# Optimization experiments

Measured on AMD Instinct MI355X. Metric: run time of the kernel, lower is better.

## Reference

```python
import jax, jax.numpy as jnp
import numpy as np

B, L, D = 16, 4096, 512


def setup_inputs() -> dict:
    key = jax.random.key(0)
    ks = jax.random.split(key, 8)
    s = 1.0 / np.sqrt(D)
    x = jax.random.normal(ks[0], (B, L, D), dtype=jnp.float32)
    Wk = jax.random.normal(ks[1], (D, D), dtype=jnp.float32) * s
    Wq = jax.random.normal(ks[2], (D, D), dtype=jnp.float32) * s
    Wv = jax.random.normal(ks[3], (D, D), dtype=jnp.float32) * s
    bk = jnp.zeros((D,), jnp.float32)
    bq = jnp.zeros((D,), jnp.float32)
    bv = jnp.zeros((D,), jnp.float32)
    lens = jax.random.randint(ks[4], (B,), 1, L + 1, dtype=jnp.int32)
    return {"x": x, "Wk": Wk, "bk": bk, "Wq": Wq, "bq": bq,
            "Wv": Wv, "bv": bv, "lens": lens}


def reference(x, Wk, bk, Wq, bq, Wv, bv, lens):
    # Dropout is identity in eval mode.
    x_k = jnp.tanh(jnp.einsum('bld,ed->ble', x, Wk) + bk)  # [B,L,D]
    x_q = jnp.tanh(jnp.einsum('bld,ed->ble', x, Wq) + bq)
    x_v = jnp.tanh(jnp.einsum('bld,ed->ble', x, Wv) + bv)
    # sum_j (x_k_i . x_q_j) == x_k_i . sum_j x_q_j  (algebraic collapse of the L x L bmm)
    q_sum = x_q.sum(axis=1)                                # [B,D]
    w = jnp.einsum('bld,bd->bl', x_k, q_sum) / (D ** 0.5)  # [B,L]
    pad = jnp.arange(L)[None, :] >= lens[:, None]          # True at padding
    w = jnp.where(pad, -jnp.inf, w)
    w = jax.nn.softmax(w, axis=1)                          # [B,L]
    # (x_v * w[...,None]).sum(-1) == x_v.sum(-1) * w
    return x_v.sum(axis=-1) * w                            # [B,L]
```

## Files before the change

### kernel.cpp

```cpp
#include <hip/hip_runtime.h>
#include <hip/hip_bf16.h>
#include <math.h>

typedef __attribute__((ext_vector_type(8))) short short8;
typedef __attribute__((ext_vector_type(16))) float f32x16;
typedef __attribute__((ext_vector_type(4))) unsigned short us4;
typedef __attribute__((ext_vector_type(8))) unsigned short us8;

static __device__ __forceinline__ unsigned short bf16_rn(float f) {
  unsigned u = __float_as_uint(f);
  u += 0x7FFFu + ((u >> 16) & 1u);
  return (unsigned short)(u >> 16);
}
static __device__ __forceinline__ void cvt_hilo(float f, unsigned short& h, unsigned short& l) {
  unsigned u = __float_as_uint(f);
  unsigned hr = u + 0x7FFFu + ((u >> 16) & 1u);
  h = (unsigned short)(hr >> 16);
  l = bf16_rn(f - __uint_as_float(hr & 0xFFFF0000u));
}
static __device__ __forceinline__ float ftanh(float x) {
  float e = __builtin_amdgcn_exp2f(x * 2.885390081777927f);
  return 1.0f - 2.0f * __builtin_amdgcn_rcpf(e + 1.0f);
}

__global__ void prep_kernel(const float* __restrict__ Wq,
                            const float* __restrict__ Wk,
                            const float* __restrict__ Wv,
                            unsigned short* __restrict__ ws_u16) {
  int id = blockIdx.x * 256 + threadIdx.x;
  int mat = id >> 15;
  int rem = id & 32767;
  int fn = rem >> 11;
  int gk = (rem >> 6) & 31;
  int ln = rem & 63;
  int e  = fn * 32 + (ln & 31);
  int d0 = gk * 16 + ((ln >> 5) << 3);
  const float* W = (mat == 0) ? Wq : (mat == 1) ? Wk : Wv;
  unsigned short* oh = ws_u16 + (size_t)mat * 524288 + (size_t)rem * 8;
  unsigned short* ol = oh + 262144;
  const float* src = W + (size_t)e * 512 + d0;
#pragma unroll
  for (int j = 0; j < 8; ++j) {
    unsigned short h, l;
    cvt_hilo(src[j], h, l);
    oh[j] = h;
    ol[j] = l;
  }
}

__global__ __launch_bounds__(512, 2) void pass1_q(
    const float* __restrict__ x,
    const unsigned short* __restrict__ bh,
    const unsigned short* __restrict__ bl,
    const float* __restrict__ bias,
    float* __restrict__ qpart) {
  __shared__ unsigned short hib[2][128 * 40];
  __shared__ unsigned short lob[2][128 * 40];

  const int tid = threadIdx.x;
  const int lane = tid & 63;
  const int w = tid >> 6;
  const int l31 = lane & 31, hs = lane >> 5;
  const int sr = tid >> 2, sc = (tid & 3) * 8;
  const float* gxr = x + (size_t)blockIdx.x * 128 * 512 + (size_t)sr * 512 + sc;

  const int aoff = l31 * 40 + hs * 8;
  const unsigned short* bhp = bh + (size_t)w * 16384 + (size_t)lane * 8;
  const unsigned short* blp = bl + (size_t)w * 16384 + (size_t)lane * 8;

  f32x16 acc[4][2] = {};

#define STAGE1(BUFI, V0, V1)                                        \
  {                                                                 \
    float tf[8] = {(V0).x, (V0).y, (V0).z, (V0).w,                  \
                   (V1).x, (V1).y, (V1).z, (V1).w};                 \
    us8 hv, lv;                                                     \
    _Pragma("unroll")                                               \
    for (int j = 0; j < 8; ++j) {                                   \
      unsigned short hh, ll;                                        \
      cvt_hilo(tf[j], hh, ll);                                      \
      hv[j] = hh; lv[j] = ll;                                       \
    }                                                               \
    *(us8*)&hib[BUFI][sr * 40 + sc] = hv;                           \
    *(us8*)&lob[BUFI][sr * 40 + sc] = lv;                           \
  }

  float4 xa0 = *(const float4*)(gxr);
  float4 xa1 = *(const float4*)(gxr + 4);
  STAGE1(0, xa0, xa1)
  float4 xb0 = *(const float4*)(gxr + 32);
  float4 xb1 = *(const float4*)(gxr + 36);
  __syncthreads();

#pragma unroll 1
  for (int c = 0; c < 16; ++c) {
    const int cur = c & 1;
    if (c < 15) { STAGE1(cur ^ 1, xb0, xb1) }
    if (c < 14) {
      xb0 = *(const float4*)(gxr + (c + 2) * 32);
      xb1 = *(const float4*)(gxr + (c + 2) * 32 + 4);
    }
    __syncthreads();

    short8 Bh[2][2], Bl[2][2];
#pragma unroll
    for (int ks = 0; ks < 2; ++ks)
#pragma unroll
      for (int nn = 0; nn < 2; ++nn) {
        const int go = nn * (8 * 16384) + (c * 2 + ks) * 512;
        Bh[ks][nn] = *(const short8*)(bhp + go);
        Bl[ks][nn] = *(const short8*)(blp + go);
      }
    const unsigned short* hc = &hib[cur][0];
    const unsigned short* lc = &lob[cur][0];
#pragma unroll
    for (int ks = 0; ks < 2; ++ks) {
      short8 ah[4], al[4];
#pragma unroll
      for (int mt = 0; mt < 4; ++mt) {
        ah[mt] = *(const short8*)(hc + aoff + mt * 1280 + ks * 16);
        al[mt] = *(const short8*)(lc + aoff + mt * 1280 + ks * 16);
      }
#pragma unroll
      for (int nn = 0; nn < 2; ++nn)
#pragma unroll
        for (int mt = 0; mt < 4; ++mt) {
          acc[mt][nn] = __builtin_amdgcn_mfma_f32_32x32x16_bf16(ah[mt], Bh[ks][nn], acc[mt][nn], 0, 0, 0);
          acc[mt][nn] = __builtin_amdgcn_mfma_f32_32x32x16_bf16(al[mt], Bh[ks][nn], acc[mt][nn], 0, 0, 0);
          acc[mt][nn] = __builtin_amdgcn_mfma_f32_32x32x16_bf16(ah[mt], Bl[ks][nn], acc[mt][nn], 0, 0, 0);
        }
    }
    __syncthreads();
  }
#undef STAGE1

  float cs[2];
#pragma unroll
  for (int nn = 0; nn < 2; ++nn) {
    float bc = bias[(w + 8 * nn) * 32 + l31];
    float s = 0.f;
#pragma unroll
    for (int mt = 0; mt < 4; ++mt)
#pragma unroll
      for (int r = 0; r < 16; ++r)
        s += ftanh(acc[mt][nn][r] + bc);
    s += __shfl_xor(s, 32);
    cs[nn] = s;
  }
  if (lane < 32) {
#pragma unroll
    for (int nn = 0; nn < 2; ++nn)
      qpart[(size_t)blockIdx.x * 512 + (w + 8 * nn) * 32 + l31] = cs[nn];
  }
}

__global__ __launch_bounds__(512, 2) void pass2_kv(
    const float* __restrict__ x,
    const unsigned short* __restrict__ kh,
    const unsigned short* __restrict__ kl,
    const unsigned short* __restrict__ vh,
    const float* __restrict__ bk,
    const float* __restrict__ bv,
    const float* __restrict__ q_sum,
    float* __restrict__ scores,
    float* __restrict__ sv) {
  __shared__ unsigned short hib[2][64 * 40];
  __shared__ unsigned short lob[2][64 * 40];
  __shared__ float redk[8][64];
  __shared__ float redv[8][64];

  const int tid = threadIdx.x;
  const int lane = tid & 63;
  const int w = tid >> 6;
  const int l31 = lane & 31, hs = lane >> 5;
  const int sr = tid >> 3, sc = (tid & 7) * 4;
  const float* gxr = x + (size_t)blockIdx.x * 64 * 512 + (size_t)sr * 512 + sc;

  const int aoff = l31 * 40 + hs * 8;
  const unsigned short* khp = kh + (size_t)w * 16384 + (size_t)lane * 8;
  const unsigned short* klp = kl + (size_t)w * 16384 + (size_t)lane * 8;
  const unsigned short* vhp = vh + (size_t)w * 16384 + (size_t)lane * 8;

  f32x16 acck[2][2] = {};
  f32x16 accv[2][2] = {};

#define STAGE2(BUFI, V)                                             \
  {                                                                 \
    float tf[4] = {(V).x, (V).y, (V).z, (V).w};                     \
    us4 hv, lv;                                                     \
    _Pragma("unroll")                                               \
    for (int j = 0; j < 4; ++j) {                                   \
      unsigned short hh, ll;                                        \
      cvt_hilo(tf[j], hh, ll);                                      \
      hv[j] = hh; lv[j] = ll;                                       \
    }                                                               \
    *(us4*)&hib[BUFI][sr * 40 + sc] = hv;                           \
    *(us4*)&lob[BUFI][sr * 40 + sc] = lv;                           \
  }

  float4 xa = *(const float4*)(gxr);
  STAGE2(0, xa)
  float4 xb = *(const float4*)(gxr + 32);
  __syncthreads();

#pragma unroll 1
  for (int c = 0; c < 16; ++c) {
    const int cur = c & 1;
    if (c < 15) { STAGE2(cur ^ 1, xb) }
    if (c < 14) { xb = *(const float4*)(gxr + (c + 2) * 32); }
    __syncthreads();

    short8 Kh[2][2], Kl[2][2], Vh[2][2];
#pragma unroll
    for (int ks = 0; ks < 2; ++ks)
#pragma unroll
      for (int nn = 0; nn < 2; ++nn) {
        const int go = nn * (8 * 16384) + (c * 2 + ks) * 512;
        Kh[ks][nn] = *(const short8*)(khp + go);
        Kl[ks][nn] = *(const short8*)(klp + go);
        Vh[ks][nn] = *(const short8*)(vhp + go);
      }
    const unsigned short* hc = &hib[cur][0];
    const unsigned short* lc = &lob[cur][0];
#pragma unroll
    for (int ks = 0; ks < 2; ++ks) {
      short8 ah[2], al[2];
#pragma unroll
      for (int mt = 0; mt < 2; ++mt) {
        ah[mt] = *(const short8*)(hc + aoff + mt * 1280 + ks * 16);
        al[mt] = *(const short8*)(lc + aoff + mt * 1280 + ks * 16);
      }
#pragma unroll
      for (int nn = 0; nn < 2; ++nn)
#pragma unroll
        for (int mt = 0; mt < 2; ++mt) {
          acck[mt][nn] = __builtin_amdgcn_mfma_f32_32x32x16_bf16(ah[mt], Kh[ks][nn], acck[mt][nn], 0, 0, 0);
          acck[mt][nn] = __builtin_amdgcn_mfma_f32_32x32x16_bf16(al[mt], Kh[ks][nn], acck[mt][nn], 0, 0, 0);
          acck[mt][nn] = __builtin_amdgcn_mfma_f32_32x32x16_bf16(ah[mt], Kl[ks][nn], acck[mt][nn], 0, 0, 0);
          accv[mt][nn] = __builtin_amdgcn_mfma_f32_32x32x16_bf16(ah[mt], Vh[ks][nn], accv[mt][nn], 0, 0, 0);
        }
    }
    __syncthreads();
  }
#undef STAGE2

  const int b = blockIdx.x >> 6;
  float qs[2], bkc[2], bvc[2];
#pragma unroll
  for (int nn = 0; nn < 2; ++nn) {
    int col = (w + 8 * nn) * 32 + l31;
    qs[nn] = q_sum[b * 512 + col];
    bkc[nn] = bk[col];
    bvc[nn] = bv[col];
  }
#pragma unroll
  for (int mt = 0; mt < 2; ++mt)
#pragma unroll
    for (int r = 0; r < 16; ++r) {
      float sk = ftanh(acck[mt][0][r] + bkc[0]) * qs[0] +
                 ftanh(acck[mt][1][r] + bkc[1]) * qs[1];
      float s_v = ftanh(accv[mt][0][r] + bvc[0]) +
                  ftanh(accv[mt][1][r] + bvc[1]);
#pragma unroll
      for (int off = 1; off <= 16; off <<= 1) {
        sk += __shfl_xor(sk, off);
        s_v += __shfl_xor(s_v, off);
      }
      if (l31 == 0) {
        int row = mt * 32 + (r & 3) + 8 * (r >> 2) + 4 * hs;
        redk[w][row] = sk;
        redv[w][row] = s_v;
      }
    }
  __syncthreads();
  if (tid < 64) {
    float s = 0.f;
#pragma unroll
    for (int j = 0; j < 8; ++j) s += redk[j][tid];
    scores[(size_t)blockIdx.x * 64 + tid] = s;
  } else if (tid < 128) {
    int r = tid - 64;
    float s = 0.f;
#pragma unroll
    for (int j = 0; j < 8; ++j) s += redv[j][r];
    sv[(size_t)blockIdx.x * 64 + r] = s;
  }
}

__global__ void reduce_q(const float* __restrict__ qpart, float* __restrict__ q_sum) {
  int b = blockIdx.x;
  int e = threadIdx.x;
  const float* p = qpart + (size_t)b * 32 * 512 + e;
  float s = 0.f;
#pragma unroll
  for (int j = 0; j < 32; ++j) s += p[j * 512];
  q_sum[b * 512 + e] = s;
}

__global__ void softmax_out(const float* __restrict__ scores,
                            const float* __restrict__ sv,
                            const int* __restrict__ lens,
                            float* __restrict__ out) {
  const int b = blockIdx.x;
  const int tid = threadIdx.x;
  const int lane = tid & 63, wid = tid >> 6;
  const int len = lens[b];
  const float scale = 0.04419417382415922f;
  __shared__ float sb[4];
  __shared__ float sb2[4];

  float sreg[16];
  const float* sc = scores + (size_t)b * 4096;
#pragma unroll
  for (int j = 0; j < 16; ++j) sreg[j] = sc[tid + j * 256] * scale;

  float m = -1e30f;
#pragma unroll
  for (int j = 0; j < 16; ++j)
    if (tid + j * 256 < len) m = fmaxf(m, sreg[j]);
#pragma unroll
  for (int off = 32; off >= 1; off >>= 1) m = fmaxf(m, __shfl_xor(m, off));
  if (lane == 0) sb[wid] = m;
  __syncthreads();
  m = fmaxf(fmaxf(sb[0], sb[1]), fmaxf(sb[2], sb[3]));

  float s = 0.f;
#pragma unroll
  for (int j = 0; j < 16; ++j)
    if (tid + j * 256 < len) s += expf(sreg[j] - m);
#pragma unroll
  for (int off = 32; off >= 1; off >>= 1) s += __shfl_xor(s, off);
  if (lane == 0) sb2[wid] = s;
  __syncthreads();
  const float inv = 1.f / (sb2[0] + sb2[1] + sb2[2] + sb2[3]);

  const float* svb = sv + (size_t)b * 4096;
  float* ob = out + (size_t)b * 4096;
#pragma unroll
  for (int j = 0; j < 16; ++j) {
    int l = tid + j * 256;
    ob[l] = (l < len) ? svb[l] * expf(sreg[j] - m) * inv : 0.0f;
  }
}

extern "C" void kernel_launch(void* const* d_in, const int* in_sizes, int n_in,
                              void* d_out, int out_size, void* d_ws, size_t ws_size,
                              hipStream_t stream) {
  const float* x  = (const float*)d_in[0];
  const float* Wk = (const float*)d_in[1];
  const float* bk = (const float*)d_in[2];
  const float* Wq = (const float*)d_in[3];
  const float* bq = (const float*)d_in[4];
  const float* Wv = (const float*)d_in[5];
  const float* bv = (const float*)d_in[6];
  const int* lens = (const int*)d_in[7];
  float* out = (float*)d_out;

  char* ws = (char*)d_ws;
  unsigned short* wfu = (unsigned short*)ws;
  const size_t WQ_HI = 0, WQ_LO = 262144;
  const size_t WK_HI = 524288, WK_LO = 786432;
  const size_t WV_HI = 1048576;
  float* qpart  = (float*)(ws + 3u * 1024 * 1024);
  float* q_sum  = (float*)(ws + 5u * 1024 * 1024);
  float* sv     = (float*)(ws + 5u * 1024 * 1024 + 32768);
  float* scores = (float*)(ws + 5u * 1024 * 1024 + 32768 + 262144);

  prep_kernel<<<384, 256, 0, stream>>>(Wq, Wk, Wv, wfu);
  pass1_q<<<512, 512, 0, stream>>>(x, wfu + WQ_HI, wfu + WQ_LO, bq, qpart);
  reduce_q<<<16, 512, 0, stream>>>(qpart, q_sum);
  pass2_kv<<<1024, 512, 0, stream>>>(x, wfu + WK_HI, wfu + WK_LO, wfu + WV_HI,
                                     bk, bv, q_sum, scores, sv);
  softmax_out<<<16, 256, 0, stream>>>(scores, sv, lens, out);
}
```

Before: 271.9 us.

## Use triple-buffered LDS staging to drop one barrier per k-chunk

Both GEMM passes move from double-buffered to triple-buffered LDS tiles for the hi/lo bf16 split of x. The trailing __syncthreads in each k-loop iteration is removed. The conversion and store of the next chunk now happen after the weight loads and overlap with the MFMAs on the current buffer. This costs 50% more LDS per block, which may limit occupancy with two 512-thread blocks per CU, and the reordered global loads could change latency hiding.

New measurement: 263.3 us. 3.2% less time.

```diff
diff --git a/kernel.cpp b/kernel.cpp
--- a/kernel.cpp
+++ b/kernel.cpp
@@ -54,8 +54,8 @@
     const unsigned short* __restrict__ bl,
     const float* __restrict__ bias,
     float* __restrict__ qpart) {
-  __shared__ unsigned short hib[2][128 * 40];
-  __shared__ unsigned short lob[2][128 * 40];
+  __shared__ unsigned short hib[3][128 * 40];
+  __shared__ unsigned short lob[3][128 * 40];
 
   const int tid = threadIdx.x;
   const int lane = tid & 63;
@@ -85,23 +85,17 @@
     *(us8*)&lob[BUFI][sr * 40 + sc] = lv;                           \
   }
 
-  float4 xa0 = *(const float4*)(gxr);
-  float4 xa1 = *(const float4*)(gxr + 4);
-  STAGE1(0, xa0, xa1)
-  float4 xb0 = *(const float4*)(gxr + 32);
-  float4 xb1 = *(const float4*)(gxr + 36);
-  __syncthreads();
-
+  float4 xs0 = *(const float4*)(gxr);
+  float4 xs1 = *(const float4*)(gxr + 4);
+  STAGE1(0, xs0, xs1)
+  xs0 = *(const float4*)(gxr + 32);
+  xs1 = *(const float4*)(gxr + 36);
+
+  int cur = 0;
 #pragma unroll 1
   for (int c = 0; c < 16; ++c) {
-    const int cur = c & 1;
-    if (c < 15) { STAGE1(cur ^ 1, xb0, xb1) }
-    if (c < 14) {
-      xb0 = *(const float4*)(gxr + (c + 2) * 32);
-      xb1 = *(const float4*)(gxr + (c + 2) * 32 + 4);
-    }
+    const int nxt = (cur == 2) ? 0 : cur + 1;
     __syncthreads();
-
     short8 Bh[2][2], Bl[2][2];
 #pragma unroll
     for (int ks = 0; ks < 2; ++ks)
@@ -111,6 +105,13 @@
         Bh[ks][nn] = *(const short8*)(bhp + go);
         Bl[ks][nn] = *(const short8*)(blp + go);
       }
+    float4 xn0 = xs0, xn1 = xs1;
+    if (c < 14) {
+      xn0 = *(const float4*)(gxr + (c + 2) * 32);
+      xn1 = *(const float4*)(gxr + (c + 2) * 32 + 4);
+    }
+    if (c < 15) { STAGE1(nxt, xs0, xs1) }
+
     const unsigned short* hc = &hib[cur][0];
     const unsigned short* lc = &lob[cur][0];
 #pragma unroll
@@ -130,7 +131,8 @@
           acc[mt][nn] = __builtin_amdgcn_mfma_f32_32x32x16_bf16(ah[mt], Bl[ks][nn], acc[mt][nn], 0, 0, 0);
         }
     }
-    __syncthreads();
+    xs0 = xn0; xs1 = xn1;
+    cur = nxt;
   }
 #undef STAGE1
 
@@ -164,8 +166,8 @@
     const float* __restrict__ q_sum,
     float* __restrict__ scores,
     float* __restrict__ sv) {
-  __shared__ unsigned short hib[2][64 * 40];
-  __shared__ unsigned short lob[2][64 * 40];
+  __shared__ unsigned short hib[3][64 * 40];
+  __shared__ unsigned short lob[3][64 * 40];
   __shared__ float redk[8][64];
   __shared__ float redv[8][64];
 
@@ -198,18 +200,15 @@
     *(us4*)&lob[BUFI][sr * 40 + sc] = lv;                           \
   }
 
-  float4 xa = *(const float4*)(gxr);
-  STAGE2(0, xa)
-  float4 xb = *(const float4*)(gxr + 32);
-  __syncthreads();
-
+  float4 xs = *(const float4*)(gxr);
+  STAGE2(0, xs)
+  xs = *(const float4*)(gxr + 32);
+
+  int cur = 0;
 #pragma unroll 1
   for (int c = 0; c < 16; ++c) {
-    const int cur = c & 1;
-    if (c < 15) { STAGE2(cur ^ 1, xb) }
-    if (c < 14) { xb = *(const float4*)(gxr + (c + 2) * 32); }
+    const int nxt = (cur == 2) ? 0 : cur + 1;
     __syncthreads();
-
     short8 Kh[2][2], Kl[2][2], Vh[2][2];
 #pragma unroll
     for (int ks = 0; ks < 2; ++ks)
@@ -220,6 +219,10 @@
         Kl[ks][nn] = *(const short8*)(klp + go);
         Vh[ks][nn] = *(const short8*)(vhp + go);
       }
+    float4 xn = xs;
+    if (c < 14) { xn = *(const float4*)(gxr + (c + 2) * 32); }
+    if (c < 15) { STAGE2(nxt, xs) }
+
     const unsigned short* hc = &hib[cur][0];
     const unsigned short* lc = &lob[cur][0];
 #pragma unroll
@@ -240,7 +243,8 @@
           accv[mt][nn] = __builtin_amdgcn_mfma_f32_32x32x16_bf16(ah[mt], Vh[ks][nn], accv[mt][nn], 0, 0, 0);
         }
     }
-    __syncthreads();
+    xs = xn;
+    cur = nxt;
   }
 #undef STAGE2
 
```

## Stage full-K 32-row x tile in LDS and stream weights per wave

Applied to the files above, without the earlier changes.

Both GEMM passes now load a whole 32x512 row tile of x into LDS up front (hi/lo bf16 split, padded stride) and then run the full K loop with no per-chunk barriers. Each of 4 waves owns 4 output column tiles and streams weight fragments straight from global memory. Blocks shrink to 256 threads and grids grow to 2048, which gives more independent blocks and removes the double-buffer synchronisation. In exchange, weight reuse per block drops because each block covers only 32 rows, so weight traffic from L2 rises, and the LDS footprint per block grows.

Result: slower. 453.4 us (+66.7%).

```diff
diff --git a/kernel.cpp b/kernel.cpp
--- a/kernel.cpp
+++ b/kernel.cpp
@@ -2,10 +2,11 @@
 #include <hip/hip_bf16.h>
 #include <math.h>
 
+#define LSTRIDE 520
+
 typedef __attribute__((ext_vector_type(8))) short short8;
 typedef __attribute__((ext_vector_type(16))) float f32x16;
 typedef __attribute__((ext_vector_type(4))) unsigned short us4;
-typedef __attribute__((ext_vector_type(8))) unsigned short us8;
 
 static __device__ __forceinline__ unsigned short bf16_rn(float f) {
   unsigned u = __float_as_uint(f);
@@ -48,113 +49,80 @@
   }
 }
 
-__global__ __launch_bounds__(512, 2) void pass1_q(
+#define STAGE_TILE(GX)                                                      \
+  {                                                                         \
+    const int row = tid >> 3, cb = (tid & 7) * 4;                           \
+    const float* gsrc = (GX) + (size_t)row * 512 + cb;                      \
+    unsigned short* hd = &hib[row * LSTRIDE + cb];                          \
+    unsigned short* ld = &lob[row * LSTRIDE + cb];                          \
+    _Pragma("unroll")                                                       \
+    for (int j = 0; j < 16; ++j) {                                          \
+      float4 v = *(const float4*)(gsrc + j * 32);                           \
+      us4 hv, lv;                                                           \
+      unsigned short hh, ll;                                                \
+      cvt_hilo(v.x, hh, ll); hv[0] = hh; lv[0] = ll;                        \
+      cvt_hilo(v.y, hh, ll); hv[1] = hh; lv[1] = ll;                        \
+      cvt_hilo(v.z, hh, ll); hv[2] = hh; lv[2] = ll;                        \
+      cvt_hilo(v.w, hh, ll); hv[3] = hh; lv[3] = ll;                        \
+      *(us4*)(hd + j * 32) = hv;                                            \
+      *(us4*)(ld + j * 32) = lv;                                            \
+    }                                                                       \
+  }
+
+__global__ __launch_bounds__(256, 2) void pass1_q(
     const float* __restrict__ x,
     const unsigned short* __restrict__ bh,
     const unsigned short* __restrict__ bl,
     const float* __restrict__ bias,
     float* __restrict__ qpart) {
-  __shared__ unsigned short hib[2][128 * 40];
-  __shared__ unsigned short lob[2][128 * 40];
+  __shared__ unsigned short hib[32 * LSTRIDE];
+  __shared__ unsigned short lob[32 * LSTRIDE];
 
   const int tid = threadIdx.x;
   const int lane = tid & 63;
   const int w = tid >> 6;
   const int l31 = lane & 31, hs = lane >> 5;
-  const int sr = tid >> 2, sc = (tid & 3) * 8;
-  const float* gxr = x + (size_t)blockIdx.x * 128 * 512 + (size_t)sr * 512 + sc;
-
-  const int aoff = l31 * 40 + hs * 8;
-  const unsigned short* bhp = bh + (size_t)w * 16384 + (size_t)lane * 8;
-  const unsigned short* blp = bl + (size_t)w * 16384 + (size_t)lane * 8;
-
-  f32x16 acc[4][2] = {};
-
-#define STAGE1(BUFI, V0, V1)                                        \
-  {                                                                 \
-    float tf[8] = {(V0).x, (V0).y, (V0).z, (V0).w,                  \
-                   (V1).x, (V1).y, (V1).z, (V1).w};                 \
-    us8 hv, lv;                                                     \
-    _Pragma("unroll")                                               \
-    for (int j = 0; j < 8; ++j) {                                   \
-      unsigned short hh, ll;                                        \
-      cvt_hilo(tf[j], hh, ll);                                      \
-      hv[j] = hh; lv[j] = ll;                                       \
-    }                                                               \
-    *(us8*)&hib[BUFI][sr * 40 + sc] = hv;                           \
-    *(us8*)&lob[BUFI][sr * 40 + sc] = lv;                           \
-  }
-
-  float4 xa0 = *(const float4*)(gxr);
-  float4 xa1 = *(const float4*)(gxr + 4);
-  STAGE1(0, xa0, xa1)
-  float4 xb0 = *(const float4*)(gxr + 32);
-  float4 xb1 = *(const float4*)(gxr + 36);
-  __syncthreads();
-
-#pragma unroll 1
-  for (int c = 0; c < 16; ++c) {
-    const int cur = c & 1;
-    if (c < 15) { STAGE1(cur ^ 1, xb0, xb1) }
-    if (c < 14) {
-      xb0 = *(const float4*)(gxr + (c + 2) * 32);
-      xb1 = *(const float4*)(gxr + (c + 2) * 32 + 4);
-    }
-    __syncthreads();
-
-    short8 Bh[2][2], Bl[2][2];
-#pragma unroll
-    for (int ks = 0; ks < 2; ++ks)
-#pragma unroll
-      for (int nn = 0; nn < 2; ++nn) {
-        const int go = nn * (8 * 16384) + (c * 2 + ks) * 512;
-        Bh[ks][nn] = *(const short8*)(bhp + go);
-        Bl[ks][nn] = *(const short8*)(blp + go);
+
+  STAGE_TILE(x + (size_t)blockIdx.x * 32 * 512)
+  __syncthreads();
+
+  const unsigned short* bhp = bh + (size_t)lane * 8;
+  const unsigned short* blp = bl + (size_t)lane * 8;
+  const int abase = l31 * LSTRIDE + hs * 8;
+
+  f32x16 acc[4] = {};
+#pragma unroll 4
+  for (int kc = 0; kc < 16; ++kc) {
+#pragma unroll
+    for (int ks = 0; ks < 2; ++ks) {
+      short8 ah = *(const short8*)&hib[abase + kc * 32 + ks * 16];
+      short8 al = *(const short8*)&lob[abase + kc * 32 + ks * 16];
+      const int gk = kc * 2 + ks;
+#pragma unroll
+      for (int i = 0; i < 4; ++i) {
+        const int bo = ((w + i * 4) * 32 + gk) * 512;
+        short8 Bh = *(const short8*)(bhp + bo);
+        short8 Bl = *(const short8*)(blp + bo);
+        acc[i] = __builtin_amdgcn_mfma_f32_32x32x16_bf16(ah, Bh, acc[i], 0, 0, 0);
+        acc[i] = __builtin_amdgcn_mfma_f32_32x32x16_bf16(al, Bh, acc[i], 0, 0, 0);
+        acc[i] = __builtin_amdgcn_mfma_f32_32x32x16_bf16(ah, Bl, acc[i], 0, 0, 0);
       }
-    const unsigned short* hc = &hib[cur][0];
-    const unsigned short* lc = &lob[cur][0];
-#pragma unroll
-    for (int ks = 0; ks < 2; ++ks) {
-      short8 ah[4], al[4];
-#pragma unroll
-      for (int mt = 0; mt < 4; ++mt) {
-        ah[mt] = *(const short8*)(hc + aoff + mt * 1280 + ks * 16);
-        al[mt] = *(const short8*)(lc + aoff + mt * 1280 + ks * 16);
-      }
-#pragma unroll
-      for (int nn = 0; nn < 2; ++nn)
-#pragma unroll
-        for (int mt = 0; mt < 4; ++mt) {
-          acc[mt][nn] = __builtin_amdgcn_mfma_f32_32x32x16_bf16(ah[mt], Bh[ks][nn], acc[mt][nn], 0, 0, 0);
-          acc[mt][nn] = __builtin_amdgcn_mfma_f32_32x32x16_bf16(al[mt], Bh[ks][nn], acc[mt][nn], 0, 0, 0);
-          acc[mt][nn] = __builtin_amdgcn_mfma_f32_32x32x16_bf16(ah[mt], Bl[ks][nn], acc[mt][nn], 0, 0, 0);
-        }
-    }
-    __syncthreads();
-  }
-#undef STAGE1
-
-  float cs[2];
-#pragma unroll
-  for (int nn = 0; nn < 2; ++nn) {
-    float bc = bias[(w + 8 * nn) * 32 + l31];
+    }
+  }
+
+#pragma unroll
+  for (int i = 0; i < 4; ++i) {
+    const int n = w + i * 4;
+    float bc = bias[n * 32 + l31];
     float s = 0.f;
 #pragma unroll
-    for (int mt = 0; mt < 4; ++mt)
-#pragma unroll
-      for (int r = 0; r < 16; ++r)
-        s += ftanh(acc[mt][nn][r] + bc);
+    for (int r = 0; r < 16; ++r) s += ftanh(acc[i][r] + bc);
     s += __shfl_xor(s, 32);
-    cs[nn] = s;
-  }
-  if (lane < 32) {
-#pragma unroll
-    for (int nn = 0; nn < 2; ++nn)
-      qpart[(size_t)blockIdx.x * 512 + (w + 8 * nn) * 32 + l31] = cs[nn];
-  }
-}
-
-__global__ __launch_bounds__(512, 2) void pass2_kv(
+    if (lane < 32) qpart[(size_t)blockIdx.x * 512 + n * 32 + l31] = s;
+  }
+}
+
+__global__ __launch_bounds__(256, 2) void pass2_kv(
     const float* __restrict__ x,
     const unsigned short* __restrict__ kh,
     const unsigned short* __restrict__ kl,
@@ -164,137 +132,99 @@
     const float* __restrict__ q_sum,
     float* __restrict__ scores,
     float* __restrict__ sv) {
-  __shared__ unsigned short hib[2][64 * 40];
-  __shared__ unsigned short lob[2][64 * 40];
-  __shared__ float redk[8][64];
-  __shared__ float redv[8][64];
+  __shared__ unsigned short hib[32 * LSTRIDE];
+  __shared__ unsigned short lob[32 * LSTRIDE];
+  __shared__ float redk[4][32];
+  __shared__ float redv[4][32];
 
   const int tid = threadIdx.x;
   const int lane = tid & 63;
   const int w = tid >> 6;
   const int l31 = lane & 31, hs = lane >> 5;
-  const int sr = tid >> 3, sc = (tid & 7) * 4;
-  const float* gxr = x + (size_t)blockIdx.x * 64 * 512 + (size_t)sr * 512 + sc;
-
-  const int aoff = l31 * 40 + hs * 8;
-  const unsigned short* khp = kh + (size_t)w * 16384 + (size_t)lane * 8;
-  const unsigned short* klp = kl + (size_t)w * 16384 + (size_t)lane * 8;
-  const unsigned short* vhp = vh + (size_t)w * 16384 + (size_t)lane * 8;
-
-  f32x16 acck[2][2] = {};
-  f32x16 accv[2][2] = {};
-
-#define STAGE2(BUFI, V)                                             \
-  {                                                                 \
-    float tf[4] = {(V).x, (V).y, (V).z, (V).w};                     \
-    us4 hv, lv;                                                     \
-    _Pragma("unroll")                                               \
-    for (int j = 0; j < 4; ++j) {                                   \
-      unsigned short hh, ll;                                        \
-      cvt_hilo(tf[j], hh, ll);                                      \
-      hv[j] = hh; lv[j] = ll;                                       \
-    }                                                               \
-    *(us4*)&hib[BUFI][sr * 40 + sc] = hv;                           \
-    *(us4*)&lob[BUFI][sr * 40 + sc] = lv;                           \
-  }
-
-  float4 xa = *(const float4*)(gxr);
-  STAGE2(0, xa)
-  float4 xb = *(const float4*)(gxr + 32);
-  __syncthreads();
-
-#pragma unroll 1
-  for (int c = 0; c < 16; ++c) {
-    const int cur = c & 1;
-    if (c < 15) { STAGE2(cur ^ 1, xb) }
-    if (c < 14) { xb = *(const float4*)(gxr + (c + 2) * 32); }
-    __syncthreads();
-
-    short8 Kh[2][2], Kl[2][2], Vh[2][2];
-#pragma unroll
-    for (int ks = 0; ks < 2; ++ks)
-#pragma unroll
-      for (int nn = 0; nn < 2; ++nn) {
-        const int go = nn * (8 * 16384) + (c * 2 + ks) * 512;
-        Kh[ks][nn] = *(const short8*)(khp + go);
-        Kl[ks][nn] = *(const short8*)(klp + go);
-        Vh[ks][nn] = *(const short8*)(vhp + go);
+
+  STAGE_TILE(x + (size_t)blockIdx.x * 32 * 512)
+  __syncthreads();
+
+  const unsigned short* khp = kh + (size_t)lane * 8;
+  const unsigned short* klp = kl + (size_t)lane * 8;
+  const unsigned short* vhp = vh + (size_t)lane * 8;
+  const int abase = l31 * LSTRIDE + hs * 8;
+
+  f32x16 acck[4] = {};
+  f32x16 accv[4] = {};
+#pragma unroll 4
+  for (int kc = 0; kc < 16; ++kc) {
+#pragma unroll
+    for (int ks = 0; ks < 2; ++ks) {
+      short8 ah = *(const short8*)&hib[abase + kc * 32 + ks * 16];
+      short8 al = *(const short8*)&lob[abase + kc * 32 + ks * 16];
+      const int gk = kc * 2 + ks;
+#pragma unroll
+      for (int i = 0; i < 4; ++i) {
+        const int bo = ((w + i * 4) * 32 + gk) * 512;
+        short8 Kh = *(const short8*)(khp + bo);
+        short8 Kl = *(const short8*)(klp + bo);
+        short8 Vh = *(const short8*)(vhp + bo);
+        acck[i] = __builtin_amdgcn_mfma_f32_32x32x16_bf16(ah, Kh, acck[i], 0, 0, 0);
+        acck[i] = __builtin_amdgcn_mfma_f32_32x32x16_bf16(al, Kh, acck[i], 0, 0, 0);
+        acck[i] = __builtin_amdgcn_mfma_f32_32x32x16_bf16(ah, Kl, acck[i], 0, 0, 0);
+        accv[i] = __builtin_amdgcn_mfma_f32_32x32x16_bf16(ah, Vh, accv[i], 0, 0, 0);
       }
-    const unsigned short* hc = &hib[cur][0];
-    const unsigned short* lc = &lob[cur][0];
-#pragma unroll
-    for (int ks = 0; ks < 2; ++ks) {
-      short8 ah[2], al[2];
-#pragma unroll
-      for (int mt = 0; mt < 2; ++mt) {
-        ah[mt] = *(const short8*)(hc + aoff + mt * 1280 + ks * 16);
-        al[mt] = *(const short8*)(lc + aoff + mt * 1280 + ks * 16);
-      }
-#pragma unroll
-      for (int nn = 0; nn < 2; ++nn)
-#pragma unroll
-        for (int mt = 0; mt < 2; ++mt) {
-          acck[mt][nn] = __builtin_amdgcn_mfma_f32_32x32x16_bf16(ah[mt], Kh[ks][nn], acck[mt][nn], 0, 0, 0);
-          acck[mt][nn] = __builtin_amdgcn_mfma_f32_32x32x16_bf16(al[mt], Kh[ks][nn], acck[mt][nn], 0, 0, 0);
-          acck[mt][nn] = __builtin_amdgcn_mfma_f32_32x32x16_bf16(ah[mt], Kl[ks][nn], acck[mt][nn], 0, 0, 0);
-          accv[mt][nn] = __builtin_amdgcn_mfma_f32_32x32x16_bf16(ah[mt], Vh[ks][nn], accv[mt][nn], 0, 0, 0);
-        }
-    }
-    __syncthreads();
-  }
-#undef STAGE2
-
-  const int b = blockIdx.x >> 6;
-  float qs[2], bkc[2], bvc[2];
-#pragma unroll
-  for (int nn = 0; nn < 2; ++nn) {
-    int col = (w + 8 * nn) * 32 + l31;
-    qs[nn] = q_sum[b * 512 + col];
-    bkc[nn] = bk[col];
-    bvc[nn] = bv[col];
-  }
-#pragma unroll
-  for (int mt = 0; mt < 2; ++mt)
-#pragma unroll
-    for (int r = 0; r < 16; ++r) {
-      float sk = ftanh(acck[mt][0][r] + bkc[0]) * qs[0] +
-                 ftanh(acck[mt][1][r] + bkc[1]) * qs[1];
-      float s_v = ftanh(accv[mt][0][r] + bvc[0]) +
-                  ftanh(accv[mt][1][r] + bvc[1]);
-#pragma unroll
-      for (int off = 1; off <= 16; off <<= 1) {
-        sk += __shfl_xor(sk, off);
-        s_v += __shfl_xor(s_v, off);
-      }
-      if (l31 == 0) {
-        int row = mt * 32 + (r & 3) + 8 * (r >> 2) + 4 * hs;
-        redk[w][row] = sk;
-        redv[w][row] = s_v;
-      }
-    }
-  __syncthreads();
-  if (tid < 64) {
-    float s = 0.f;
-#pragma unroll
-    for (int j = 0; j < 8; ++j) s += redk[j][tid];
-    scores[(size_t)blockIdx.x * 64 + tid] = s;
-  } else if (tid < 128) {
-    int r = tid - 64;
-    float s = 0.f;
-#pragma unroll
-    for (int j = 0; j < 8; ++j) s += redv[j][r];
-    sv[(size_t)blockIdx.x * 64 + r] = s;
+    }
+  }
+
+  const int b = blockIdx.x >> 7;
+  float qs[4], bkc[4], bvc[4];
+#pragma unroll
+  for (int i = 0; i < 4; ++i) {
+    const int col = (w + i * 4) * 32 + l31;
+    qs[i] = q_sum[b * 512 + col];
+    bkc[i] = bk[col];
+    bvc[i] = bv[col];
+  }
+#pragma unroll
+  for (int r = 0; r < 16; ++r) {
+    float a = 0.f, vs = 0.f;
+#pragma unroll
+    for (int i = 0; i < 4; ++i) {
+      a += ftanh(acck[i][r] + bkc[i]) * qs[i];
+      vs += ftanh(accv[i][r] + bvc[i]);
+    }
+#pragma unroll
+    for (int off = 1; off <= 16; off <<= 1) {
+      a += __shfl_xor(a, off);
+      vs += __shfl_xor(vs, off);
+    }
+    if (l31 == 0) {
+      const int row = (r & 3) + 8 * (r >> 2) + 4 * hs;
+      redk[w][row] = a;
+      redv[w][row] = vs;
+    }
+  }
+  __syncthreads();
+  if (tid < 32) {
+    scores[(size_t)blockIdx.x * 32 + tid] =
+        redk[0][tid] + redk[1][tid] + redk[2][tid] + redk[3][tid];
+  } else if (tid < 64) {
+    const int r = tid - 32;
+    sv[(size_t)blockIdx.x * 32 + r] =
+        redv[0][r] + redv[1][r] + redv[2][r] + redv[3][r];
   }
 }
 
 __global__ void reduce_q(const float* __restrict__ qpart, float* __restrict__ q_sum) {
   int b = blockIdx.x;
   int e = threadIdx.x;
-  const float* p = qpart + (size_t)b * 32 * 512 + e;
-  float s = 0.f;
-#pragma unroll
-  for (int j = 0; j < 32; ++j) s += p[j * 512];
-  q_sum[b * 512 + e] = s;
+  const float* p = qpart + (size_t)b * 128 * 512 + e;
+  float s0 = 0.f, s1 = 0.f, s2 = 0.f, s3 = 0.f;
+#pragma unroll 4
+  for (int j = 0; j < 128; j += 4) {
+    s0 += p[j * 512];
+    s1 += p[(j + 1) * 512];
+    s2 += p[(j + 2) * 512];
+    s3 += p[(j + 3) * 512];
+  }
+  q_sum[b * 512 + e] = (s0 + s1) + (s2 + s3);
 }
 
 __global__ void softmax_out(const float* __restrict__ scores,
@@ -362,14 +292,14 @@
   const size_t WK_HI = 524288, WK_LO = 786432;
   const size_t WV_HI = 1048576;
   float* qpart  = (float*)(ws + 3u * 1024 * 1024);
-  float* q_sum  = (float*)(ws + 5u * 1024 * 1024);
-  float* sv     = (float*)(ws + 5u * 1024 * 1024 + 32768);
-  float* scores = (float*)(ws + 5u * 1024 * 1024 + 32768 + 262144);
+  float* q_sum  = (float*)(ws + 7u * 1024 * 1024);
+  float* sv     = (float*)(ws + 7u * 1024 * 1024 + 32768);
+  float* scores = (float*)(ws + 7u * 1024 * 1024 + 32768 + 262144);
 
   prep_kernel<<<384, 256, 0, stream>>>(Wq, Wk, Wv, wfu);
-  pass1_q<<<512, 512, 0, stream>>>(x, wfu + WQ_HI, wfu + WQ_LO, bq, qpart);
+  pass1_q<<<2048, 256, 0, stream>>>(x, wfu + WQ_HI, wfu + WQ_LO, bq, qpart);
   reduce_q<<<16, 512, 0, stream>>>(qpart, q_sum);
-  pass2_kv<<<1024, 512, 0, stream>>>(x, wfu + WK_HI, wfu + WK_LO, wfu + WV_HI,
+  pass2_kv<<<2048, 256, 0, stream>>>(x, wfu + WK_HI, wfu + WK_LO, wfu + WV_HI,
                                      bk, bv, q_sum, scores, sv);
   softmax_out<<<16, 256, 0, stream>>>(scores, sv, lens, out);
 }
```
